# Kernel optimization log

Measured on AMD Instinct MI355X. Metric: run time of the kernel, lower is better.

Reference implementation:

```python
import jax, jax.numpy as jnp
import numpy as np
from jax import lax

V, C_IN, P = 40000, 4, 32
D, H, W = 4, 200, 200          # grid_size (200,200,4)=[X,Y,Z] -> dense (D,H,W)
HID, OUT = 64, 256
B = 2
EPS = 1e-5


def setup_inputs() -> dict:
    key = jax.random.key(0)
    ks = jax.random.split(key, 12)
    voxels = jax.random.normal(ks[0], (V, C_IN, P), dtype=jnp.float32)
    # unique occupied cells so scatter-set is order independent (faithful to last-write loop)
    rng = np.random.default_rng(0)
    lin = rng.choice(D * H * W, size=V, replace=False)
    z = lin // (H * W)
    rem = lin % (H * W)
    y = rem // W
    x = rem % W
    indices = jnp.asarray(np.stack([x, y, z], axis=1), dtype=jnp.int32)  # [V,3] = (x,y,z)
    s = 0.05
    w1 = jax.random.normal(ks[1], (HID, C_IN, 3, 3, 3), jnp.float32) * s
    b1 = jnp.zeros((HID,), jnp.float32)
    g1 = jnp.ones((HID,), jnp.float32)
    be1 = jnp.zeros((HID,), jnp.float32)
    w2 = jax.random.normal(ks[2], (HID, HID, 3, 3, 3), jnp.float32) * s
    b2 = jnp.zeros((HID,), jnp.float32)
    g2 = jnp.ones((HID,), jnp.float32)
    be2 = jnp.zeros((HID,), jnp.float32)
    wh = jax.random.normal(ks[3], (OUT, HID * D, 1, 1), jnp.float32) * s
    bh = jnp.zeros((OUT,), jnp.float32)
    return dict(voxels=voxels, indices=indices, batch_size=B,
                w1=w1, b1=b1, g1=g1, be1=be1,
                w2=w2, b2=b2, g2=g2, be2=be2, wh=wh, bh=bh)


def _conv3d(x, w, b):
    y = lax.conv_general_dilated(x, w, window_strides=(1, 1, 1), padding='SAME',
                                 dimension_numbers=('NCDHW', 'OIDHW', 'NCDHW'))
    return y + b[None, :, None, None, None]


def _bn_relu(x, g, b):
    # BatchNorm3d in training mode: biased batch stats over (N,D,H,W)
    m = x.mean(axis=(0, 2, 3, 4), keepdims=True)
    v = x.var(axis=(0, 2, 3, 4), keepdims=True)
    y = (x - m) * lax.rsqrt(v + EPS)
    y = g[None, :, None, None, None] * y + b[None, :, None, None, None]
    return jax.nn.relu(y)


def reference(voxels, indices, batch_size, w1, b1, g1, be1, w2, b2, g2, be2, wh, bh):
    # PseudoSparseConv3d: mean over points, scatter into dense grid
    feat = voxels.mean(axis=2)  # [V, C_IN]
    grid = jnp.zeros((D, H, W, C_IN), voxels.dtype)
    grid = grid.at[indices[:, 2], indices[:, 1], indices[:, 0]].set(feat)
    dense = jnp.broadcast_to(jnp.transpose(grid, (3, 0, 1, 2))[None],
                             (batch_size, C_IN, D, H, W))  # same scatter for every batch slot
    x = _bn_relu(_conv3d(dense, w1, b1), g1, be1)          # [B, HID, D, H, W]
    x = _bn_relu(_conv3d(x, w2, b2), g2, be2)              # SparseConv3d block
    # HeightPooling: [B, C, D, H, W] -> [B, C*D, H, W] -> 1x1 conv
    x = x.reshape(batch_size, HID * D, H, W)
    y = lax.conv_general_dilated(x, wh, window_strides=(1, 1), padding='SAME',
                                 dimension_numbers=('NCHW', 'OIHW', 'NCHW'))
    return y + bh[None, :, None, None]
```

## Files before the change

### kernel.cpp

```cpp
#include <hip/hip_runtime.h>


#define VN   40000
#define CIN  4
#define PN   32
#define SP2  40000
#define SP3  160000
#define HID  64
#define OUTC 256
#define EPSF 1e-5f

typedef __attribute__((ext_vector_type(8)))  short short8;
typedef __attribute__((ext_vector_type(16))) float f32x16;

__device__ inline unsigned short f2bf(float f) {
    unsigned u = __builtin_bit_cast(unsigned, f);
    return (unsigned short)((u + 0x7fffu + ((u >> 16) & 1u)) >> 16);
}
__device__ inline float bf2f(unsigned short h) {
    return __builtin_bit_cast(float, ((unsigned)h) << 16);
}
__device__ inline short8 ld8(const unsigned short* p) {
    return __builtin_bit_cast(short8, *reinterpret_cast<const uint4*>(p));
}

__global__ __launch_bounds__(256) void k_prep(const float* __restrict__ vox,
                                              const int* __restrict__ idx,
                                              const float* __restrict__ W1,
                                              const float* __restrict__ W2,
                                              const float* __restrict__ WH,
                                              unsigned short* __restrict__ G8,
                                              unsigned short* __restrict__ A1,
                                              unsigned short* __restrict__ A2,
                                              unsigned short* __restrict__ AH) {
    int i = blockIdx.x * 256 + threadIdx.x;
    if (i < VN) {
        int v = i;
        const float4* p = reinterpret_cast<const float4*>(vox + (size_t)v * CIN * PN);
        float m[4];
#pragma unroll
        for (int c = 0; c < 4; ++c) {
            float s = 0.f;
#pragma unroll
            for (int q = 0; q < PN / 4; ++q) {
                float4 r = p[c * (PN / 4) + q];
                s += (r.x + r.y) + (r.z + r.w);
            }
            m[c] = s * (1.f / PN);
        }
        int x = idx[v * 3 + 0], y = idx[v * 3 + 1], z = idx[v * 3 + 2];
        size_t sp = (size_t)z * SP2 + y * 200 + x;
        uint2 o;
        o.x = (unsigned)f2bf(m[0]) | ((unsigned)f2bf(m[1]) << 16);
        o.y = (unsigned)f2bf(m[2]) | ((unsigned)f2bf(m[3]) << 16);
        *reinterpret_cast<uint2*>(G8 + sp * 8) = o;
        return;
    }
    int k = i - VN;
    if (k < 14336) {
        int j = k & 7, l = (k >> 3) & 63, mt = (k >> 9) & 1, s = k >> 10;
        int co = mt * 32 + (l & 31);
        int tap = s * 2 + (l >> 5);
        float v = 0.f;
        if (tap < 27 && j < 4) v = W1[(co * 4 + j) * 27 + tap];
        A1[k] = f2bf(v);
    } else if (k < 124928) {
        int k2 = k - 14336;
        int j = k2 & 7, l = (k2 >> 3) & 63, mt = (k2 >> 9) & 1, cib = (k2 >> 10) & 3, tap = k2 >> 12;
        int co = mt * 32 + (l & 31);
        int ci = cib * 16 + (l >> 5) * 8 + j;
        A2[k2] = f2bf(W2[(co * 64 + ci) * 27 + tap]);
    } else if (k < 190464) {
        int k3 = k - 124928;
        int j = k3 & 7, l = (k3 >> 3) & 63, mtg = (k3 >> 9) & 7, cib = k3 >> 12;
        int o = mtg * 32 + (l & 31);
        int kp = cib * 16 + (l >> 5) * 8 + j;
        int hid = kp & 63, d = kp >> 6;
        AH[k3] = f2bf(WH[o * 256 + hid * 4 + d]);
    }
}

__global__ __launch_bounds__(128) void k_conv1m(const unsigned short* __restrict__ G8,
                                                const unsigned short* __restrict__ A1,
                                                const float* __restrict__ B1,
                                                unsigned short* __restrict__ Y1) {
    __shared__ unsigned short win[360 * 8];
    int bh = blockIdx.x / 25, bw = blockIdx.x % 25;
    int h0 = bh * 4, w0 = bw * 8;
    int t = threadIdx.x;
    for (int e = t; e < 360; e += 128) {
        int p6 = e / 60, rr = e % 60;
        int hh = rr / 10, ww = rr % 10;
        int ps = p6 - 1, hg = h0 + hh - 1, wg = w0 + ww - 1;
        uint4 v = make_uint4(0, 0, 0, 0);
        if ((unsigned)ps < 4u && (unsigned)hg < 200u && (unsigned)wg < 200u)
            v = *reinterpret_cast<const uint4*>(G8 + (size_t)(ps * SP2 + hg * 200 + wg) * 8);
        *reinterpret_cast<uint4*>(win + e * 8) = v;
    }
    __syncthreads();
    int wv = t >> 6, l = t & 63;
    int hi = l >> 5, h_off = (l & 31) >> 3, w = l & 7;
    int d0 = wv * 2;
    f32x16 acc[2][2] = {};
#pragma unroll
    for (int s = 0; s < 14; ++s) {
        int tap = s * 2 + hi; if (tap > 26) tap = 26;
        int kd = tap / 9, r9 = tap % 9, kh = r9 / 3, kw = r9 % 3;
        const uint4* ap = reinterpret_cast<const uint4*>(A1) + (s * 2) * 64 + l;
        short8 a0 = __builtin_bit_cast(short8, ap[0]);
        short8 a1 = __builtin_bit_cast(short8, ap[64]);
#pragma unroll
        for (int nt = 0; nt < 2; ++nt) {
            int cell = (d0 + nt + kd) * 60 + (h_off + kh) * 10 + (w + kw);
            short8 bfr = ld8(win + cell * 8);
            acc[0][nt] = __builtin_amdgcn_mfma_f32_32x32x16_bf16(a0, bfr, acc[0][nt], 0, 0, 0);
            acc[1][nt] = __builtin_amdgcn_mfma_f32_32x32x16_bf16(a1, bfr, acc[1][nt], 0, 0, 0);
        }
    }
    const float4* Bv = reinterpret_cast<const float4*>(B1);
#pragma unroll
    for (int mt = 0; mt < 2; ++mt) {
#pragma unroll
        for (int nt = 0; nt < 2; ++nt) {
            int sp = (d0 + nt) * SP2 + (h0 + h_off) * 200 + (w0 + w);
#pragma unroll
            for (int rq = 0; rq < 4; ++rq) {
                int co0 = mt * 32 + rq * 8 + hi * 4;
                float4 bb = Bv[co0 >> 2];
                uint2 o;
                o.x = (unsigned)f2bf(acc[mt][nt][rq * 4 + 0] + bb.x) |
                      ((unsigned)f2bf(acc[mt][nt][rq * 4 + 1] + bb.y) << 16);
                o.y = (unsigned)f2bf(acc[mt][nt][rq * 4 + 2] + bb.z) |
                      ((unsigned)f2bf(acc[mt][nt][rq * 4 + 3] + bb.w) << 16);
                *reinterpret_cast<uint2*>(Y1 + (size_t)sp * 64 + co0) = o;
            }
        }
    }
}

__global__ __launch_bounds__(128, 2) void k_conv2m(const unsigned short* __restrict__ X,
                                                   const unsigned short* __restrict__ A2,
                                                   const float* __restrict__ AB1,
                                                   const float* __restrict__ B2,
                                                   unsigned short* __restrict__ Y2) {
    __shared__ unsigned short win[240 * 72];
    int bh = blockIdx.x / 25, bw = blockIdx.x % 25;
    int h0 = bh * 4, w0 = bw * 8;
    int t = threadIdx.x;
    int s8 = (t & 7) * 8;
    float a8[8], b8[8];
#pragma unroll
    for (int j = 0; j < 8; ++j) { a8[j] = AB1[s8 + j]; b8[j] = AB1[64 + s8 + j]; }
#pragma unroll
    for (int i = 0; i < 15; ++i) {
        int cell = i * 16 + (t >> 3);
        int p = cell / 60, rr = cell % 60;
        int hh = rr / 10, ww = rr % 10;
        int hg = h0 + hh - 1, wg = w0 + ww - 1;
        uint4 st = make_uint4(0, 0, 0, 0);
        if ((unsigned)hg < 200u && (unsigned)wg < 200u) {
            uint4 raw = *reinterpret_cast<const uint4*>(X + (size_t)(p * SP2 + hg * 200 + wg) * 64 + s8);
            unsigned r[4] = {raw.x, raw.y, raw.z, raw.w};
            unsigned q[4];
#pragma unroll
            for (int k = 0; k < 4; ++k) {
                float lo = bf2f((unsigned short)(r[k] & 0xffff));
                float hv = bf2f((unsigned short)(r[k] >> 16));
                lo = fmaxf(fmaf(a8[k * 2], lo, b8[k * 2]), 0.f);
                hv = fmaxf(fmaf(a8[k * 2 + 1], hv, b8[k * 2 + 1]), 0.f);
                q[k] = (unsigned)f2bf(lo) | ((unsigned)f2bf(hv) << 16);
            }
            st = make_uint4(q[0], q[1], q[2], q[3]);
        }
        *reinterpret_cast<uint4*>(win + cell * 72 + (t & 7) * 8) = st;
    }
    __syncthreads();
    int wv = t >> 6, l = t & 63;
    int hi = l >> 5, h_off = (l & 31) >> 3, w = l & 7;
    int d0 = wv * 2;
    f32x16 acc[2][2] = {};
    for (int kd = 0; kd < 3; ++kd) {
        int p0 = d0 + kd - 1;
        bool v0 = (unsigned)p0 < 4u;
        bool v1 = (unsigned)(p0 + 1) < 4u;
#pragma unroll
        for (int khw = 0; khw < 9; ++khw) {
            int kh = khw / 3, kw = khw % 3;
            int tap = kd * 9 + khw;
            int rowc = (h_off + kh) * 10 + (w + kw);
            int cell0 = p0 * 60 + rowc;
            int cell1 = cell0 + 60;
#pragma unroll
            for (int cib = 0; cib < 4; ++cib) {
                const uint4* ap = reinterpret_cast<const uint4*>(A2) + ((tap * 4 + cib) * 2) * 64 + l;
                short8 a0 = __builtin_bit_cast(short8, ap[0]);
                short8 a1 = __builtin_bit_cast(short8, ap[64]);
                int kch = cib * 2 + hi;
                if (v0) {
                    short8 b0 = ld8(win + cell0 * 72 + kch * 8);
                    acc[0][0] = __builtin_amdgcn_mfma_f32_32x32x16_bf16(a0, b0, acc[0][0], 0, 0, 0);
                    acc[1][0] = __builtin_amdgcn_mfma_f32_32x32x16_bf16(a1, b0, acc[1][0], 0, 0, 0);
                }
                if (v1) {
                    short8 b1 = ld8(win + cell1 * 72 + kch * 8);
                    acc[0][1] = __builtin_amdgcn_mfma_f32_32x32x16_bf16(a0, b1, acc[0][1], 0, 0, 0);
                    acc[1][1] = __builtin_amdgcn_mfma_f32_32x32x16_bf16(a1, b1, acc[1][1], 0, 0, 0);
                }
            }
        }
    }
    const float4* Bv = reinterpret_cast<const float4*>(B2);
#pragma unroll
    for (int mt = 0; mt < 2; ++mt) {
#pragma unroll
        for (int nt = 0; nt < 2; ++nt) {
            int sp = (d0 + nt) * SP2 + (h0 + h_off) * 200 + (w0 + w);
#pragma unroll
            for (int rq = 0; rq < 4; ++rq) {
                int co0 = mt * 32 + rq * 8 + hi * 4;
                float4 bb = Bv[co0 >> 2];
                uint2 o;
                o.x = (unsigned)f2bf(acc[mt][nt][rq * 4 + 0] + bb.x) |
                      ((unsigned)f2bf(acc[mt][nt][rq * 4 + 1] + bb.y) << 16);
                o.y = (unsigned)f2bf(acc[mt][nt][rq * 4 + 2] + bb.z) |
                      ((unsigned)f2bf(acc[mt][nt][rq * 4 + 3] + bb.w) << 16);
                *reinterpret_cast<uint2*>(Y2 + (size_t)sp * 64 + co0) = o;
            }
        }
    }
}

__global__ __launch_bounds__(256) void k_stats2p(const unsigned short* __restrict__ Y,
                                                 float* __restrict__ P) {
    int bid = blockIdx.x, t = threadIdx.x, wv = t >> 6, l = t & 63;
    int cg = l & 7, rsub = l >> 3;
    float s[8] = {}, q[8] = {};
    int rend = bid * 625 + 625;
    for (int r = bid * 625 + wv * 8 + rsub; r < rend; r += 32) {
        uint4 raw = *reinterpret_cast<const uint4*>(Y + (size_t)r * 64 + cg * 8);
        unsigned rr[4] = {raw.x, raw.y, raw.z, raw.w};
#pragma unroll
        for (int k = 0; k < 4; ++k) {
            float lo = bf2f((unsigned short)(rr[k] & 0xffff));
            float hv = bf2f((unsigned short)(rr[k] >> 16));
            s[2 * k] += lo;     q[2 * k] += lo * lo;
            s[2 * k + 1] += hv; q[2 * k + 1] += hv * hv;
        }
    }
#pragma unroll
    for (int k = 0; k < 8; ++k) {
#pragma unroll
        for (int m = 8; m < 64; m <<= 1) {
            s[k] += __shfl_xor(s[k], m);
            q[k] += __shfl_xor(q[k], m);
        }
    }
    __shared__ float ls[4][128];
    if (l < 8) {
#pragma unroll
        for (int k = 0; k < 8; ++k) {
            ls[wv][cg * 8 + k] = s[k];
            ls[wv][64 + cg * 8 + k] = q[k];
        }
    }
    __syncthreads();
    if (t < 128) P[bid * 128 + t] = ls[0][t] + ls[1][t] + ls[2][t] + ls[3][t];
}

__global__ __launch_bounds__(1024) void k_statsf(const float* __restrict__ P,
                                                 const float* __restrict__ G,
                                                 const float* __restrict__ BE,
                                                 float* __restrict__ AB) {
    __shared__ float red[8][128];
    int t = threadIdx.x, c = t & 127, grp = t >> 7;
    float S = 0.f;
    for (int b = grp; b < 256; b += 8) S += P[(size_t)b * 128 + c];
    red[grp][c] = S;
    __syncthreads();
    if (t < 128) {
        float v = 0.f;
#pragma unroll
        for (int g = 0; g < 8; ++g) v += red[g][t];
        red[0][t] = v;
    }
    __syncthreads();
    if (t < 64) {
        float m = red[0][t] * (1.f / SP3);
        float var = red[0][64 + t] * (1.f / SP3) - m * m;
        float a = G[t] * rsqrtf(var + EPSF);
        AB[t] = a; AB[64 + t] = BE[t] - m * a;
    }
}

__global__ __launch_bounds__(256) void k_headm(const unsigned short* __restrict__ X,
                                               const unsigned short* __restrict__ AH,
                                               const float* __restrict__ AB2,
                                               const float* __restrict__ BH,
                                               float* __restrict__ O, int dup2) {
    __shared__ float sab[128];
    int t = threadIdx.x;
    if (t < 128) sab[t] = AB2[t];
    __syncthreads();
    int wv = t >> 6, l = t & 63, khalf = l >> 5;
    int coh = wv >> 1, colh = wv & 1;
    int sp = blockIdx.x * 64 + colh * 32 + (l & 31);
    f32x16 acc[4] = {};
#pragma unroll
    for (int cib = 0; cib < 16; ++cib) {
        int d = cib >> 2, ch0 = (cib & 3) * 16 + khalf * 8;
        uint4 raw = *(const uint4*)(X + ((size_t)(d * SP2 + sp)) * 64 + ch0);
        unsigned r[4] = {raw.x, raw.y, raw.z, raw.w}, qq[4];
#pragma unroll
        for (int k2 = 0; k2 < 4; ++k2) {
            int c0 = ch0 + k2 * 2;
            float lo = bf2f((unsigned short)(r[k2] & 0xffff));
            float hi = bf2f((unsigned short)(r[k2] >> 16));
            lo = fmaxf(fmaf(sab[c0], lo, sab[64 + c0]), 0.f);
            hi = fmaxf(fmaf(sab[c0 + 1], hi, sab[64 + c0 + 1]), 0.f);
            qq[k2] = (unsigned)f2bf(lo) | ((unsigned)f2bf(hi) << 16);
        }
        short8 bfr = __builtin_bit_cast(short8, make_uint4(qq[0], qq[1], qq[2], qq[3]));
#pragma unroll
        for (int mi = 0; mi < 4; ++mi) {
            const uint4* ap = (const uint4*)AH + (cib * 8 + coh * 4 + mi) * 64 + l;
            short8 afr = __builtin_bit_cast(short8, *ap);
            acc[mi] = __builtin_amdgcn_mfma_f32_32x32x16_bf16(afr, bfr, acc[mi], 0, 0, 0);
        }
    }
#pragma unroll
    for (int mi = 0; mi < 4; ++mi) {
#pragma unroll
        for (int rq = 0; rq < 4; ++rq) {
            int co0 = coh * 128 + mi * 32 + rq * 8 + khalf * 4;
            float4 bb = *(const float4*)(BH + co0);
#pragma unroll
            for (int j = 0; j < 4; ++j) {
                float val = acc[mi][rq * 4 + j] + ((const float*)&bb)[j];
                size_t o = (size_t)(co0 + j) * SP2 + sp;
                O[o] = val;
                if (dup2) O[10240000 + o] = val;
            }
        }
    }
}

__global__ __launch_bounds__(256) void k_dup(float* __restrict__ O) {
    int i = blockIdx.x * 256 + threadIdx.x;
    float4* p = reinterpret_cast<float4*>(O);
    p[OUTC * SP2 / 4 + i] = p[i];
}

extern "C" void kernel_launch(void* const* d_in, const int* in_sizes, int n_in,
                              void* d_out, int out_size, void* d_ws, size_t ws_size,
                              hipStream_t stream) {
    const float* vox = (const float*)d_in[0];
    const int*   idx = (const int*)d_in[1];
    const float* w1  = (const float*)d_in[3];
    const float* b1  = (const float*)d_in[4];
    const float* g1  = (const float*)d_in[5];
    const float* be1 = (const float*)d_in[6];
    const float* w2  = (const float*)d_in[7];
    const float* b2  = (const float*)d_in[8];
    const float* g2  = (const float*)d_in[9];
    const float* be2 = (const float*)d_in[10];
    const float* wh  = (const float*)d_in[11];
    const float* bh  = (const float*)d_in[12];

    float* out = (float*)d_out;
    char* ws = (char*)d_ws;
    unsigned short* grid8  = (unsigned short*)ws;
    float*          ab1    = (float*)(ws + 2560000);
    float*          ab2    = (float*)(ws + 2560512);
    float*          part   = (float*)(ws + 2561024);
    unsigned short* apack1 = (unsigned short*)(ws + 2692096);
    unsigned short* apack2 = (unsigned short*)(ws + 2720768);
    unsigned short* apackh = (unsigned short*)(ws + 2941952);

    bool ws_mode = ws_size >= 44033024u;
    unsigned short* y1b, * y2b;
    if (ws_mode) {
        y1b = (unsigned short*)(ws + 3073024);
        y2b = (unsigned short*)(ws + 23553024);
    } else {
        y1b = (unsigned short*)(out + 10240000);
        y2b = y1b + 10240000;
    }

    hipMemsetAsync(grid8, 0, 2560000, stream);
    k_prep<<<901, 256, 0, stream>>>(vox, idx, w1, w2, wh, grid8, apack1, apack2, apackh);
    k_conv1m<<<1250, 128, 0, stream>>>(grid8, apack1, b1, y1b);
    k_stats2p<<<256, 256, 0, stream>>>(y1b, part);
    k_statsf<<<1, 1024, 0, stream>>>(part, g1, be1, ab1);
    k_conv2m<<<1250, 128, 0, stream>>>(y1b, apack2, ab1, b2, y2b);
    k_stats2p<<<256, 256, 0, stream>>>(y2b, part);
    k_statsf<<<1, 1024, 0, stream>>>(part, g2, be2, ab2);
    k_headm<<<625, 256, 0, stream>>>(y2b, apackh, ab2, bh, out, ws_mode ? 1 : 0);
    if (!ws_mode)
        k_dup<<<10000, 256, 0, stream>>>(out);
}
```

Measured before the change: 169.6 us.

## Enlarge conv2 tile to 8x8 with swizzled LDS window and split channels across waves

The second conv kernel now processes an 8x8 spatial tile per block with 256 threads and a 400-cell LDS window, which cuts the halo overhead per output and halves the block count. Waves split the 64 output channels into two halves, and each wave covers two depth slices and two row groups. The padded LDS rows (stride 72) are replaced by an XOR swizzle to avoid bank conflicts without padding. The memset is also replaced with a small zeroing kernel. In exchange, LDS use and register pressure per block go up, and with only 625 blocks occupancy may be lower.

```diff
diff --git a/kernel.cpp b/kernel.cpp
--- a/kernel.cpp
+++ b/kernel.cpp
@@ -22,6 +22,10 @@
 }
 __device__ inline short8 ld8(const unsigned short* p) {
     return __builtin_bit_cast(short8, *reinterpret_cast<const uint4*>(p));
+}
+
+__global__ __launch_bounds__(256) void k_zero(uint4* __restrict__ p) {
+    p[blockIdx.x * 256 + threadIdx.x] = make_uint4(0, 0, 0, 0);
 }
 
 __global__ __launch_bounds__(256) void k_prep(const float* __restrict__ vox,
@@ -138,46 +142,50 @@
     }
 }
 
-__global__ __launch_bounds__(128, 2) void k_conv2m(const unsigned short* __restrict__ X,
+__global__ __launch_bounds__(256, 3) void k_conv2m(const unsigned short* __restrict__ X,
                                                    const unsigned short* __restrict__ A2,
                                                    const float* __restrict__ AB1,
                                                    const float* __restrict__ B2,
                                                    unsigned short* __restrict__ Y2) {
-    __shared__ unsigned short win[240 * 72];
+    __shared__ unsigned short win[400 * 64];
     int bh = blockIdx.x / 25, bw = blockIdx.x % 25;
-    int h0 = bh * 4, w0 = bw * 8;
+    int h0 = bh * 8, w0 = bw * 8;
     int t = threadIdx.x;
     int s8 = (t & 7) * 8;
     float a8[8], b8[8];
 #pragma unroll
     for (int j = 0; j < 8; ++j) { a8[j] = AB1[s8 + j]; b8[j] = AB1[64 + s8 + j]; }
 #pragma unroll
-    for (int i = 0; i < 15; ++i) {
-        int cell = i * 16 + (t >> 3);
-        int p = cell / 60, rr = cell % 60;
-        int hh = rr / 10, ww = rr % 10;
-        int hg = h0 + hh - 1, wg = w0 + ww - 1;
-        uint4 st = make_uint4(0, 0, 0, 0);
-        if ((unsigned)hg < 200u && (unsigned)wg < 200u) {
-            uint4 raw = *reinterpret_cast<const uint4*>(X + (size_t)(p * SP2 + hg * 200 + wg) * 64 + s8);
-            unsigned r[4] = {raw.x, raw.y, raw.z, raw.w};
-            unsigned q[4];
-#pragma unroll
-            for (int k = 0; k < 4; ++k) {
-                float lo = bf2f((unsigned short)(r[k] & 0xffff));
-                float hv = bf2f((unsigned short)(r[k] >> 16));
-                lo = fmaxf(fmaf(a8[k * 2], lo, b8[k * 2]), 0.f);
-                hv = fmaxf(fmaf(a8[k * 2 + 1], hv, b8[k * 2 + 1]), 0.f);
-                q[k] = (unsigned)f2bf(lo) | ((unsigned)f2bf(hv) << 16);
-            }
-            st = make_uint4(q[0], q[1], q[2], q[3]);
-        }
-        *reinterpret_cast<uint4*>(win + cell * 72 + (t & 7) * 8) = st;
+    for (int i = 0; i < 13; ++i) {
+        int cell = i * 32 + (t >> 3);
+        if (cell < 400) {
+            int p = cell / 100, rr = cell % 100;
+            int hh = rr / 10, ww = rr % 10;
+            int hg = h0 + hh - 1, wg = w0 + ww - 1;
+            uint4 st = make_uint4(0, 0, 0, 0);
+            if ((unsigned)hg < 200u && (unsigned)wg < 200u) {
+                uint4 raw = *reinterpret_cast<const uint4*>(X + (size_t)(p * SP2 + hg * 200 + wg) * 64 + s8);
+                unsigned r[4] = {raw.x, raw.y, raw.z, raw.w};
+                unsigned q[4];
+#pragma unroll
+                for (int k = 0; k < 4; ++k) {
+                    float lo = bf2f((unsigned short)(r[k] & 0xffff));
+                    float hv = bf2f((unsigned short)(r[k] >> 16));
+                    lo = fmaxf(fmaf(a8[k * 2], lo, b8[k * 2]), 0.f);
+                    hv = fmaxf(fmaf(a8[k * 2 + 1], hv, b8[k * 2 + 1]), 0.f);
+                    q[k] = (unsigned)f2bf(lo) | ((unsigned)f2bf(hv) << 16);
+                }
+                st = make_uint4(q[0], q[1], q[2], q[3]);
+            }
+            int slot = (t & 7) ^ (cell & 7);
+            *reinterpret_cast<uint4*>(win + cell * 64 + slot * 8) = st;
+        }
     }
     __syncthreads();
     int wv = t >> 6, l = t & 63;
-    int hi = l >> 5, h_off = (l & 31) >> 3, w = l & 7;
-    int d0 = wv * 2;
+    int hi = l >> 5, hb = (l & 31) >> 3, w = l & 7;
+    int ch = wv & 1;
+    int d0 = (wv >> 1) * 2;
     f32x16 acc[2][2] = {};
     for (int kd = 0; kd < 3; ++kd) {
         int p0 = d0 + kd - 1;
@@ -187,43 +195,46 @@
         for (int khw = 0; khw < 9; ++khw) {
             int kh = khw / 3, kw = khw % 3;
             int tap = kd * 9 + khw;
-            int rowc = (h_off + kh) * 10 + (w + kw);
-            int cell0 = p0 * 60 + rowc;
-            int cell1 = cell0 + 60;
+            int rc = (hb + kh) * 10 + (w + kw);
 #pragma unroll
             for (int cib = 0; cib < 4; ++cib) {
-                const uint4* ap = reinterpret_cast<const uint4*>(A2) + ((tap * 4 + cib) * 2) * 64 + l;
-                short8 a0 = __builtin_bit_cast(short8, ap[0]);
-                short8 a1 = __builtin_bit_cast(short8, ap[64]);
+                const uint4* ap = reinterpret_cast<const uint4*>(A2) + (((tap * 4 + cib) * 2) + ch) * 64 + l;
+                short8 a = __builtin_bit_cast(short8, ap[0]);
                 int kch = cib * 2 + hi;
                 if (v0) {
-                    short8 b0 = ld8(win + cell0 * 72 + kch * 8);
-                    acc[0][0] = __builtin_amdgcn_mfma_f32_32x32x16_bf16(a0, b0, acc[0][0], 0, 0, 0);
-                    acc[1][0] = __builtin_amdgcn_mfma_f32_32x32x16_bf16(a1, b0, acc[1][0], 0, 0, 0);
+                    int c0 = p0 * 100 + rc;
+                    int c1 = c0 + 40;
+                    short8 b0 = ld8(win + c0 * 64 + ((kch ^ (c0 & 7)) << 3));
+                    short8 b1 = ld8(win + c1 * 64 + ((kch ^ (c1 & 7)) << 3));
+                    acc[0][0] = __builtin_amdgcn_mfma_f32_32x32x16_bf16(a, b0, acc[0][0], 0, 0, 0);
+                    acc[0][1] = __builtin_amdgcn_mfma_f32_32x32x16_bf16(a, b1, acc[0][1], 0, 0, 0);
                 }
                 if (v1) {
-                    short8 b1 = ld8(win + cell1 * 72 + kch * 8);
-                    acc[0][1] = __builtin_amdgcn_mfma_f32_32x32x16_bf16(a0, b1, acc[0][1], 0, 0, 0);
-                    acc[1][1] = __builtin_amdgcn_mfma_f32_32x32x16_bf16(a1, b1, acc[1][1], 0, 0, 0);
+                    int c0 = (p0 + 1) * 100 + rc;
+                    int c1 = c0 + 40;
+                    short8 b0 = ld8(win + c0 * 64 + ((kch ^ (c0 & 7)) << 3));
+                    short8 b1 = ld8(win + c1 * 64 + ((kch ^ (c1 & 7)) << 3));
+                    acc[1][0] = __builtin_amdgcn_mfma_f32_32x32x16_bf16(a, b0, acc[1][0], 0, 0, 0);
+                    acc[1][1] = __builtin_amdgcn_mfma_f32_32x32x16_bf16(a, b1, acc[1][1], 0, 0, 0);
                 }
             }
         }
     }
     const float4* Bv = reinterpret_cast<const float4*>(B2);
 #pragma unroll
-    for (int mt = 0; mt < 2; ++mt) {
-#pragma unroll
-        for (int nt = 0; nt < 2; ++nt) {
-            int sp = (d0 + nt) * SP2 + (h0 + h_off) * 200 + (w0 + w);
+    for (int nt = 0; nt < 2; ++nt) {
+#pragma unroll
+        for (int ng = 0; ng < 2; ++ng) {
+            int sp = (d0 + nt) * SP2 + (h0 + hb + ng * 4) * 200 + (w0 + w);
 #pragma unroll
             for (int rq = 0; rq < 4; ++rq) {
-                int co0 = mt * 32 + rq * 8 + hi * 4;
+                int co0 = ch * 32 + rq * 8 + hi * 4;
                 float4 bb = Bv[co0 >> 2];
                 uint2 o;
-                o.x = (unsigned)f2bf(acc[mt][nt][rq * 4 + 0] + bb.x) |
-                      ((unsigned)f2bf(acc[mt][nt][rq * 4 + 1] + bb.y) << 16);
-                o.y = (unsigned)f2bf(acc[mt][nt][rq * 4 + 2] + bb.z) |
-                      ((unsigned)f2bf(acc[mt][nt][rq * 4 + 3] + bb.w) << 16);
+                o.x = (unsigned)f2bf(acc[nt][ng][rq * 4 + 0] + bb.x) |
+                      ((unsigned)f2bf(acc[nt][ng][rq * 4 + 1] + bb.y) << 16);
+                o.y = (unsigned)f2bf(acc[nt][ng][rq * 4 + 2] + bb.z) |
+                      ((unsigned)f2bf(acc[nt][ng][rq * 4 + 3] + bb.w) << 16);
                 *reinterpret_cast<uint2*>(Y2 + (size_t)sp * 64 + co0) = o;
             }
         }
@@ -386,12 +397,12 @@
         y2b = y1b + 10240000;
     }
 
-    hipMemsetAsync(grid8, 0, 2560000, stream);
+    k_zero<<<625, 256, 0, stream>>>((uint4*)grid8);
     k_prep<<<901, 256, 0, stream>>>(vox, idx, w1, w2, wh, grid8, apack1, apack2, apackh);
     k_conv1m<<<1250, 128, 0, stream>>>(grid8, apack1, b1, y1b);
     k_stats2p<<<256, 256, 0, stream>>>(y1b, part);
     k_statsf<<<1, 1024, 0, stream>>>(part, g1, be1, ab1);
-    k_conv2m<<<1250, 128, 0, stream>>>(y1b, apack2, ab1, b2, y2b);
+    k_conv2m<<<625, 256, 0, stream>>>(y1b, apack2, ab1, b2, y2b);
     k_stats2p<<<256, 256, 0, stream>>>(y2b, part);
     k_statsf<<<1, 1024, 0, stream>>>(part, g2, be2, ab2);
     k_headm<<<625, 256, 0, stream>>>(y2b, apackh, ab2, bh, out, ws_mode ? 1 : 0);
```

New measurement: 144.0 us. -15.1%, faster.
